# Kernel optimization log

Measured on AMD Instinct MI355X. Metric: run time of the kernel, lower is better.

## Reference

```python
import jax, jax.numpy as jnp
import numpy as np

B, D, E, H, C = 16384, 512, 16, 2048, 1
LN_EPS = 1e-5


def setup_inputs() -> dict:
    key = jax.random.key(0)
    ks = jax.random.split(key, 6)
    scale = 0.02
    return {
        "z": jax.random.normal(ks[0], (B, D), jnp.float32),
        "gate_w": jax.random.normal(ks[1], (D, E), jnp.float32) * scale,
        "gate_b": jnp.zeros((E,), jnp.float32),
        "ln_scale": jnp.ones((E, D), jnp.float32),
        "ln_bias": jnp.zeros((E, D), jnp.float32),
        "w1": jax.random.normal(ks[2], (E, D, H), jnp.float32) * scale,
        "b1": jnp.zeros((E, H), jnp.float32),
        "w2": jax.random.normal(ks[3], (E, H, C), jnp.float32) * scale,
        "b2": jnp.zeros((E, C), jnp.float32),
    }


def reference(z, gate_w, gate_b, ln_scale, ln_bias, w1, b1, w2, b2):
    # Gate: softmax over experts, top-1 routing by argmax
    g = jax.nn.softmax(z @ gate_w + gate_b, axis=-1)  # (B, E)
    idx = jnp.argmax(g, axis=-1)                      # (B,)

    # LayerNorm statistics are expert-independent (affine differs per expert)
    mu = jnp.mean(z, axis=-1, keepdims=True)
    var = jnp.mean(jnp.square(z - mu), axis=-1, keepdims=True)
    zn = (z - mu) / jnp.sqrt(var + LN_EPS)            # (B, D)

    # Loop over the small fixed expert set; combine by top-1 mask.
    logits = jnp.zeros((z.shape[0],), z.dtype)
    for e in range(E):
        x = zn * ln_scale[e] + ln_bias[e]                       # (B, D)
        h = jax.nn.gelu(x @ w1[e] + b1[e], approximate=False)   # (B, H)
        o = jnp.squeeze(h @ w2[e] + b2[e], axis=-1)             # (B,) since C==1
        logits = jnp.where(idx == e, o, logits)
    return logits, g
```

## Files before the change

### kernel.cpp

```cpp
#include <hip/hip_runtime.h>
#include <math.h>

#define NB 16384
#define ND 512
#define NE 16
#define NH 2048
#define BM 128
#define BN 128
#define BK 64
#define NCH (NH / BN)
#define NTB 8
#define LN_EPS 1e-5f

typedef __attribute__((ext_vector_type(8))) short s8v;
typedef __attribute__((ext_vector_type(4))) float f4v;

#define WS_W1T_OFF  ((size_t)0)
#define WS_W1T_BYTES ((size_t)NE * NH * ND * 2)
#define WS_XN_OFF   (WS_W1T_OFF + WS_W1T_BYTES)
#define WS_XN_BYTES ((size_t)NB * ND * 2)
#define WS_IDX_OFF  (WS_XN_OFF + WS_XN_BYTES)
#define WS_CNT_OFF  (WS_IDX_OFF + (size_t)NB * 4)
#define WS_ROWS_OFF (WS_CNT_OFF + 256)

__device__ __forceinline__ unsigned short bf16_rne(float f) {
    unsigned u = __float_as_uint(f);
    unsigned r = (u + 0x7fffu + ((u >> 16) & 1u)) >> 16;
    return (unsigned short)r;
}

__global__ __launch_bounds__(256) void w1conv_kernel(
    const float* __restrict__ w1, unsigned short* __restrict__ w1t)
{
    int bid = blockIdx.x;
    int e = bid & 15;
    int rest = bid >> 4;
    int db = rest & 7;
    int hb = rest >> 3;
    int h = hb * 256 + threadIdx.x;

    const float* src = w1 + ((size_t)e * ND + db * 64) * NH + h;
    unsigned int u[32];
#pragma unroll
    for (int p = 0; p < 32; ++p) {
        float f0 = src[(size_t)(2 * p) * NH];
        float f1 = src[(size_t)(2 * p + 1) * NH];
        u[p] = (unsigned)bf16_rne(f0) | ((unsigned)bf16_rne(f1) << 16);
    }
    uint4* dst = reinterpret_cast<uint4*>(
        w1t + ((size_t)e * NH + h) * ND + db * 64);
#pragma unroll
    for (int p = 0; p < 8; ++p)
        dst[p] = make_uint4(u[4 * p], u[4 * p + 1], u[4 * p + 2], u[4 * p + 3]);
}

__global__ __launch_bounds__(256) void gate_ln_kernel(
    const float* __restrict__ z, const float* __restrict__ gw,
    const float* __restrict__ gb, const float* __restrict__ ln_s,
    const float* __restrict__ ln_b, const float* __restrict__ b2,
    unsigned short* __restrict__ xn, int* __restrict__ idx_ws,
    float* __restrict__ g_out, float* __restrict__ logits)
{
    int wave = threadIdx.x >> 6;
    int lane = threadIdx.x & 63;
    int b = blockIdx.x * 4 + wave;
    int q = lane & 3, dg = lane >> 2;

    const float* zr = z + (size_t)b * ND;
    float4 zv[8];
#pragma unroll
    for (int i = 0; i < 8; ++i)
        zv[i] = *reinterpret_cast<const float4*>(zr + dg * 32 + i * 4);

    float sum = 0.f, ssq = 0.f;
    float ga[4] = {0.f, 0.f, 0.f, 0.f};
#pragma unroll
    for (int i = 0; i < 8; ++i) {
        float zs[4] = {zv[i].x, zv[i].y, zv[i].z, zv[i].w};
#pragma unroll
        for (int t = 0; t < 4; ++t) {
            int d = dg * 32 + i * 4 + t;
            float4 w4 = *reinterpret_cast<const float4*>(gw + (size_t)d * NE + q * 4);
            ga[0] = fmaf(zs[t], w4.x, ga[0]);
            ga[1] = fmaf(zs[t], w4.y, ga[1]);
            ga[2] = fmaf(zs[t], w4.z, ga[2]);
            ga[3] = fmaf(zs[t], w4.w, ga[3]);
            sum += zs[t];
            ssq = fmaf(zs[t], zs[t], ssq);
        }
    }
#pragma unroll
    for (int m = 4; m <= 32; m <<= 1) {
        sum += __shfl_xor(sum, m);
        ssq += __shfl_xor(ssq, m);
#pragma unroll
        for (int j = 0; j < 4; ++j) ga[j] += __shfl_xor(ga[j], m);
    }
#pragma unroll
    for (int j = 0; j < 4; ++j) ga[j] += gb[q * 4 + j];

    float mu = sum * (1.f / ND);
    float var = ssq * (1.f / ND) - mu * mu;
    float rstd = rsqrtf(var + LN_EPS);

    float lmax = fmaxf(fmaxf(ga[0], ga[1]), fmaxf(ga[2], ga[3]));
    lmax = fmaxf(lmax, __shfl_xor(lmax, 1));
    lmax = fmaxf(lmax, __shfl_xor(lmax, 2));
    float ge[4], lsum = 0.f;
#pragma unroll
    for (int j = 0; j < 4; ++j) { ge[j] = __expf(ga[j] - lmax); lsum += ge[j]; }
    lsum += __shfl_xor(lsum, 1);
    lsum += __shfl_xor(lsum, 2);
    float rden = 1.f / lsum;

    int li = 1000;
#pragma unroll
    for (int j = 3; j >= 0; --j) if (ga[j] == lmax) li = q * 4 + j;
    li = min(li, __shfl_xor(li, 1));
    li = min(li, __shfl_xor(li, 2));

    float gv0 = ge[0] * rden, gv1 = ge[1] * rden;
    float gv2 = ge[2] * rden, gv3 = ge[3] * rden;
    int srcl = lane >> 2;
    float t0 = __shfl(gv0, srcl), t1 = __shfl(gv1, srcl);
    float t2 = __shfl(gv2, srcl), t3 = __shfl(gv3, srcl);
    float gval = (q == 0) ? t0 : (q == 1) ? t1 : (q == 2) ? t2 : t3;
    if (lane < NE) g_out[(size_t)b * NE + lane] = gval;

    float4 xa, xc;
    if (q == 0)      { xa = zv[0]; xc = zv[1]; }
    else if (q == 1) { xa = zv[2]; xc = zv[3]; }
    else if (q == 2) { xa = zv[4]; xc = zv[5]; }
    else             { xa = zv[6]; xc = zv[7]; }
    int dofs = dg * 32 + q * 8;
    const float* ls = ln_s + (size_t)li * ND + dofs;
    const float* lb = ln_b + (size_t)li * ND + dofs;
    float4 s0 = *reinterpret_cast<const float4*>(ls);
    float4 s1 = *reinterpret_cast<const float4*>(ls + 4);
    float4 u0 = *reinterpret_cast<const float4*>(lb);
    float4 u1 = *reinterpret_cast<const float4*>(lb + 4);
    unsigned short xb[8];
    xb[0] = bf16_rne((xa.x - mu) * rstd * s0.x + u0.x);
    xb[1] = bf16_rne((xa.y - mu) * rstd * s0.y + u0.y);
    xb[2] = bf16_rne((xa.z - mu) * rstd * s0.z + u0.z);
    xb[3] = bf16_rne((xa.w - mu) * rstd * s0.w + u0.w);
    xb[4] = bf16_rne((xc.x - mu) * rstd * s1.x + u1.x);
    xb[5] = bf16_rne((xc.y - mu) * rstd * s1.y + u1.y);
    xb[6] = bf16_rne((xc.z - mu) * rstd * s1.z + u1.z);
    xb[7] = bf16_rne((xc.w - mu) * rstd * s1.w + u1.w);
    *reinterpret_cast<s8v*>(xn + (size_t)b * ND + dofs) =
        *reinterpret_cast<s8v*>(xb);

    if (lane == 0) {
        idx_ws[b] = li;
        logits[b] = b2[li];
    }
}

__global__ __launch_bounds__(256) void bucket_kernel(
    const int* __restrict__ idx_ws, int* __restrict__ counts,
    int* __restrict__ rows)
{
    __shared__ int qc[4];
    int e = blockIdx.x;
    int tid = threadIdx.x, w = tid >> 6, lane = tid & 63;
    const int4* p = reinterpret_cast<const int4*>(idx_ws) + (size_t)w * 1024;

    int c = 0;
#pragma unroll 4
    for (int it = 0; it < 16; ++it) {
        int4 v = p[it * 64 + lane];
        c += (v.x == e) + (v.y == e) + (v.z == e) + (v.w == e);
    }
#pragma unroll
    for (int m = 1; m < 64; m <<= 1) c += __shfl_xor(c, m);
    if (lane == 0) qc[w] = c;
    __syncthreads();

    int base = 0;
    for (int j = 0; j < w; ++j) base += qc[j];
    unsigned long long below = (lane == 0) ? 0ull : ((~0ull) >> (64 - lane));
    int* re = rows + (size_t)e * NB;
    int run = base;
#pragma unroll 2
    for (int it = 0; it < 16; ++it) {
        int4 v = p[it * 64 + lane];
        int vv[4] = {v.x, v.y, v.z, v.w};
#pragma unroll
        for (int k = 0; k < 4; ++k) {
            unsigned long long m = __ballot(vv[k] == e);
            if (vv[k] == e)
                re[run + __popcll(m & below)] = w * 4096 + (it * 64 + lane) * 4 + k;
            run += __popcll(m);
        }
    }
    if (tid == 0) counts[e] = qc[0] + qc[1] + qc[2] + qc[3];
}

__global__ __launch_bounds__(256, 2) void mfma_mlp(
    const unsigned short* __restrict__ xn, const unsigned short* __restrict__ w1t,
    const float* __restrict__ b1, const float* __restrict__ w2,
    const int* __restrict__ counts, const int* __restrict__ rows,
    float* __restrict__ logits)
{
    __shared__ unsigned short A_lds[2][BM * BK];
    __shared__ unsigned short B_lds[2][BN * BK];

    int bid = blockIdx.x;
    int e = bid & 15;
    int rest = bid >> 4;
    int ch = rest & 15;
    int tb0 = rest >> 4;
    int c0 = ch * BN;
    int tid = threadIdx.x, lane = tid & 63, wave = tid >> 6;
    int wm = wave & 1, wn = wave >> 1;
    int cnt = counts[e];
    const int* rl = rows + (size_t)e * NB;

    int rquad = lane >> 3;
    int sbyte = ((lane & 7) * 16) ^ (rquad << 4);

    size_t boff[4];
#pragma unroll
    for (int i = 0; i < 4; ++i) {
        int cl = (wave * 4 + i) * 8 + rquad;
        boff[i] = ((size_t)(e * NH + c0 + cl) * ND) * 2 + sbyte;
    }

    float b1v[4], w2v[4];
#pragma unroll
    for (int cf = 0; cf < 4; ++cf) {
        int col = c0 + wn * 64 + cf * 16 + (lane & 15);
        b1v[cf] = b1[(size_t)e * NH + col];
        w2v[cf] = w2[(size_t)e * NH + col];
    }

    int g = lane >> 4;
    int fr = lane & 15;
    int sw = (lane & 7) << 4;
    int aoffs[4], boffs[4];
#pragma unroll
    for (int f = 0; f < 4; ++f) {
        aoffs[f] = (wm * 64 + f * 16 + fr) * 128;
        boffs[f] = (wn * 64 + f * 16 + fr) * 128;
    }

    for (int tb = tb0; tb * BM < cnt; tb += NTB) {
        int rbase = tb * BM;

        size_t aoff[4];
#pragma unroll
        for (int i = 0; i < 4; ++i) {
            int rloc = (wave * 4 + i) * 8 + rquad;
            int rg = rl[min(rbase + rloc, cnt - 1)];
            aoff[i] = (size_t)rg * (ND * 2) + sbyte;
        }

#pragma unroll
        for (int i = 0; i < 4; ++i) {
            __builtin_amdgcn_global_load_lds(
                (const __attribute__((address_space(1))) void*)((const char*)xn + aoff[i]),
                (__attribute__((address_space(3))) void*)&A_lds[0][(wave * 4 + i) * 8 * BK],
                16, 0, 0);
            __builtin_amdgcn_global_load_lds(
                (const __attribute__((address_space(1))) void*)((const char*)w1t + boff[i]),
                (__attribute__((address_space(3))) void*)&B_lds[0][(wave * 4 + i) * 8 * BK],
                16, 0, 0);
        }
        __syncthreads();

        f4v acc[4][4];
#pragma unroll
        for (int rf = 0; rf < 4; ++rf)
#pragma unroll
            for (int cf = 0; cf < 4; ++cf) acc[rf][cf] = (f4v){0.f, 0.f, 0.f, 0.f};

#pragma unroll
        for (int s = 0; s < 8; ++s) {
            int cb = s & 1;
            if (s < 7) {
#pragma unroll
                for (int i = 0; i < 4; ++i) {
                    __builtin_amdgcn_global_load_lds(
                        (const __attribute__((address_space(1))) void*)
                            ((const char*)xn + aoff[i] + (s + 1) * 128),
                        (__attribute__((address_space(3))) void*)
                            &A_lds[cb ^ 1][(wave * 4 + i) * 8 * BK],
                        16, 0, 0);
                    __builtin_amdgcn_global_load_lds(
                        (const __attribute__((address_space(1))) void*)
                            ((const char*)w1t + boff[i] + (s + 1) * 128),
                        (__attribute__((address_space(3))) void*)
                            &B_lds[cb ^ 1][(wave * 4 + i) * 8 * BK],
                        16, 0, 0);
                }
            }
#pragma unroll
            for (int ks = 0; ks < 2; ++ks) {
                int kb = (ks * 64 + g * 16) ^ sw;
                s8v a[4], bb[4];
#pragma unroll
                for (int rf = 0; rf < 4; ++rf)
                    a[rf] = *reinterpret_cast<const s8v*>(
                        (const char*)&A_lds[cb][0] + aoffs[rf] + kb);
#pragma unroll
                for (int cf = 0; cf < 4; ++cf)
                    bb[cf] = *reinterpret_cast<const s8v*>(
                        (const char*)&B_lds[cb][0] + boffs[cf] + kb);
#pragma unroll
                for (int rf = 0; rf < 4; ++rf)
#pragma unroll
                    for (int cf = 0; cf < 4; ++cf)
                        acc[rf][cf] = __builtin_amdgcn_mfma_f32_16x16x32_bf16(
                            a[rf], bb[cf], acc[rf][cf], 0, 0, 0);
            }
            if (s < 7) __syncthreads();
        }

#pragma unroll
        for (int rf = 0; rf < 4; ++rf) {
            float pj[4] = {0.f, 0.f, 0.f, 0.f};
#pragma unroll
            for (int cf = 0; cf < 4; ++cf) {
#pragma unroll
                for (int j = 0; j < 4; ++j) {
                    float h = acc[rf][cf][j] + b1v[cf];
                    float uu = h * (0.7978845608f + 0.0356774081f * h * h);
                    float ex = __expf(2.f * uu);
                    float th = 1.f - 2.f / (ex + 1.f);
                    pj[j] = fmaf(0.5f * h * (1.f + th), w2v[cf], pj[j]);
                }
            }
#pragma unroll
            for (int m = 1; m < 16; m <<= 1)
#pragma unroll
                for (int j = 0; j < 4; ++j) pj[j] += __shfl_xor(pj[j], m);
            if ((lane & 15) == 0) {
#pragma unroll
                for (int j = 0; j < 4; ++j) {
                    int rloc = wm * 64 + rf * 16 + g * 4 + j;
                    if (rbase + rloc < cnt)
                        atomicAdd(&logits[rl[rbase + rloc]], pj[j]);
                }
            }
        }
    }
}

extern "C" void kernel_launch(void* const* d_in, const int* in_sizes, int n_in,
                              void* d_out, int out_size, void* d_ws, size_t ws_size,
                              hipStream_t stream) {
    const float* z    = (const float*)d_in[0];
    const float* gw   = (const float*)d_in[1];
    const float* gb   = (const float*)d_in[2];
    const float* ln_s = (const float*)d_in[3];
    const float* ln_b = (const float*)d_in[4];
    const float* w1   = (const float*)d_in[5];
    const float* b1   = (const float*)d_in[6];
    const float* w2   = (const float*)d_in[7];
    const float* b2   = (const float*)d_in[8];

    float* logits = (float*)d_out;
    float* g_out  = (float*)d_out + NB;

    char* ws = (char*)d_ws;
    unsigned short* w1t = (unsigned short*)(ws + WS_W1T_OFF);
    unsigned short* xn  = (unsigned short*)(ws + WS_XN_OFF);
    int* idx_ws = (int*)(ws + WS_IDX_OFF);
    int* cnts   = (int*)(ws + WS_CNT_OFF);
    int* rowl   = (int*)(ws + WS_ROWS_OFF);

    w1conv_kernel<<<NE * 64, 256, 0, stream>>>(w1, w1t);
    gate_ln_kernel<<<NB / 4, 256, 0, stream>>>(z, gw, gb, ln_s, ln_b, b2,
                                               xn, idx_ws, g_out, logits);
    bucket_kernel<<<NE, 256, 0, stream>>>(idx_ws, cnts, rowl);
    mfma_mlp<<<NE * NCH * NTB, 256, 0, stream>>>(xn, w1t, b1, w2, cnts, rowl,
                                                 logits);
}
```

Before: 175.3 us.

## Convert W1 to bf16 inside GEMM and pre-gather rows into contiguous buffer

Drops the separate W1 fp32-to-bf16 transpose kernel. The GEMM now loads fp32 W1 tiles into registers, converts them to bf16 and writes them into swizzled LDS, so the weight tensor is read once instead of being read and re-written. A new gather kernel copies normalized rows into an expert-sorted contiguous buffer, which removes indirect row loads inside the GEMM. The GEMM prefetches across row tiles, blocks with no work exit early, and NTB drops from 8 to 2, so each block covers more row tiles. The cost is redundant fp32 W1 reads and conversions across row-tile blocks, plus one extra gather pass.

```diff
diff --git a/kernel.cpp b/kernel.cpp
--- a/kernel.cpp
+++ b/kernel.cpp
@@ -9,17 +9,17 @@
 #define BN 128
 #define BK 64
 #define NCH (NH / BN)
-#define NTB 8
+#define NTB 2
 #define LN_EPS 1e-5f
 
 typedef __attribute__((ext_vector_type(8))) short s8v;
 typedef __attribute__((ext_vector_type(4))) float f4v;
 
-#define WS_W1T_OFF  ((size_t)0)
-#define WS_W1T_BYTES ((size_t)NE * NH * ND * 2)
-#define WS_XN_OFF   (WS_W1T_OFF + WS_W1T_BYTES)
+#define WS_XN_OFF   ((size_t)0)
 #define WS_XN_BYTES ((size_t)NB * ND * 2)
-#define WS_IDX_OFF  (WS_XN_OFF + WS_XN_BYTES)
+#define WS_XNS_OFF  (WS_XN_OFF + WS_XN_BYTES)
+#define WS_XNS_BYTES ((size_t)NB * ND * 2)
+#define WS_IDX_OFF  (WS_XNS_OFF + WS_XNS_BYTES)
 #define WS_CNT_OFF  (WS_IDX_OFF + (size_t)NB * 4)
 #define WS_ROWS_OFF (WS_CNT_OFF + 256)
 
@@ -28,30 +28,8 @@
     unsigned r = (u + 0x7fffu + ((u >> 16) & 1u)) >> 16;
     return (unsigned short)r;
 }
-
-__global__ __launch_bounds__(256) void w1conv_kernel(
-    const float* __restrict__ w1, unsigned short* __restrict__ w1t)
-{
-    int bid = blockIdx.x;
-    int e = bid & 15;
-    int rest = bid >> 4;
-    int db = rest & 7;
-    int hb = rest >> 3;
-    int h = hb * 256 + threadIdx.x;
-
-    const float* src = w1 + ((size_t)e * ND + db * 64) * NH + h;
-    unsigned int u[32];
-#pragma unroll
-    for (int p = 0; p < 32; ++p) {
-        float f0 = src[(size_t)(2 * p) * NH];
-        float f1 = src[(size_t)(2 * p + 1) * NH];
-        u[p] = (unsigned)bf16_rne(f0) | ((unsigned)bf16_rne(f1) << 16);
-    }
-    uint4* dst = reinterpret_cast<uint4*>(
-        w1t + ((size_t)e * NH + h) * ND + db * 64);
-#pragma unroll
-    for (int p = 0; p < 8; ++p)
-        dst[p] = make_uint4(u[4 * p], u[4 * p + 1], u[4 * p + 2], u[4 * p + 3]);
+__device__ __forceinline__ unsigned int pack2(float a, float b) {
+    return (unsigned)bf16_rne(a) | ((unsigned)bf16_rne(b) << 16);
 }
 
 __global__ __launch_bounds__(256) void gate_ln_kernel(
@@ -197,8 +175,26 @@
     if (tid == 0) counts[e] = qc[0] + qc[1] + qc[2] + qc[3];
 }
 
+__global__ __launch_bounds__(256) void gather_kernel(
+    const unsigned short* __restrict__ xn, const int* __restrict__ counts,
+    const int* __restrict__ rows, unsigned short* __restrict__ xns)
+{
+    int wave = threadIdx.x >> 6, lane = threadIdx.x & 63;
+    int slot = blockIdx.x * 4 + wave;
+
+    int pfx = 0, e = 0;
+#pragma unroll
+    for (int i = 0; i < NE; ++i) {
+        int c = counts[i];
+        if (e == i && slot >= pfx + c) { pfx += c; e = i + 1; }
+    }
+    int row = rows[(size_t)e * NB + (slot - pfx)];
+    s8v v = *reinterpret_cast<const s8v*>(xn + (size_t)row * ND + lane * 8);
+    *reinterpret_cast<s8v*>(xns + (size_t)slot * ND + lane * 8) = v;
+}
+
 __global__ __launch_bounds__(256, 2) void mfma_mlp(
-    const unsigned short* __restrict__ xn, const unsigned short* __restrict__ w1t,
+    const unsigned short* __restrict__ xns, const float* __restrict__ w1,
     const float* __restrict__ b1, const float* __restrict__ w2,
     const int* __restrict__ counts, const int* __restrict__ rows,
     float* __restrict__ logits)
@@ -214,18 +210,19 @@
     int c0 = ch * BN;
     int tid = threadIdx.x, lane = tid & 63, wave = tid >> 6;
     int wm = wave & 1, wn = wave >> 1;
+
     int cnt = counts[e];
+    if (tb0 * BM >= cnt) return;
+    int pfx = 0;
+    for (int i = 0; i < e; ++i) pfx += counts[i];
     const int* rl = rows + (size_t)e * NB;
 
     int rquad = lane >> 3;
     int sbyte = ((lane & 7) * 16) ^ (rquad << 4);
 
-    size_t boff[4];
-#pragma unroll
-    for (int i = 0; i < 4; ++i) {
-        int cl = (wave * 4 + i) * 8 + rquad;
-        boff[i] = ((size_t)(e * NH + c0 + cl) * ND) * 2 + sbyte;
-    }
+    int bc4 = (tid & 31) * 4;
+    int bkq = tid >> 5;
+    const float* bbase = w1 + (size_t)e * ND * NH + c0 + bc4;
 
     float b1v[4], w2v[4];
 #pragma unroll
@@ -245,30 +242,50 @@
         boffs[f] = (wn * 64 + f * 16 + fr) * 128;
     }
 
-    for (int tb = tb0; tb * BM < cnt; tb += NTB) {
+    f4v bfv[8];
+
+#define ISSUE_B(ss)                                                          \
+    {   const float* bs = bbase + (size_t)((ss) * 64 + bkq * 8) * NH;        \
+        _Pragma("unroll")                                                    \
+        for (int j = 0; j < 8; ++j)                                          \
+            bfv[j] = *reinterpret_cast<const f4v*>(bs + (size_t)j * NH); }
+
+#define ISSUE_A(buf, sbase, ss)                                              \
+    {   _Pragma("unroll")                                                    \
+        for (int i = 0; i < 4; ++i) {                                        \
+            int rloc = (wave * 4 + i) * 8 + rquad;                           \
+            int slot = min((sbase) + rloc, NB - 1);                          \
+            __builtin_amdgcn_global_load_lds(                                \
+                (const __attribute__((address_space(1))) void*)              \
+                    ((const char*)xns + (size_t)slot * 1024 + (ss) * 128 + sbyte), \
+                (__attribute__((address_space(3))) void*)                    \
+                    &A_lds[buf][(wave * 4 + i) * 8 * BK], 16, 0, 0); } }
+
+#define WRITE_B(buf)                                                         \
+    {   _Pragma("unroll")                                                    \
+        for (int i = 0; i < 4; ++i) {                                        \
+            int cc = bc4 + i;                                                \
+            int wb = cc * 128 + ((bkq * 16) ^ ((cc & 7) << 4));              \
+            *reinterpret_cast<uint4*>((char*)&B_lds[buf][0] + wb) =          \
+                make_uint4(pack2(bfv[0][i], bfv[1][i]),                      \
+                           pack2(bfv[2][i], bfv[3][i]),                      \
+                           pack2(bfv[4][i], bfv[5][i]),                      \
+                           pack2(bfv[6][i], bfv[7][i])); } }
+
+    int tb = tb0;
+    int sbase = pfx + tb * BM;
+
+    ISSUE_B(0);
+    ISSUE_A(0, sbase, 0);
+    WRITE_B(0);
+    __syncthreads();
+
+    while (true) {
+        int tbn = tb + NTB;
+        bool hasNext = (tbn * BM < cnt);
+        int sbasen = pfx + tbn * BM;
         int rbase = tb * BM;
 
-        size_t aoff[4];
-#pragma unroll
-        for (int i = 0; i < 4; ++i) {
-            int rloc = (wave * 4 + i) * 8 + rquad;
-            int rg = rl[min(rbase + rloc, cnt - 1)];
-            aoff[i] = (size_t)rg * (ND * 2) + sbyte;
-        }
-
-#pragma unroll
-        for (int i = 0; i < 4; ++i) {
-            __builtin_amdgcn_global_load_lds(
-                (const __attribute__((address_space(1))) void*)((const char*)xn + aoff[i]),
-                (__attribute__((address_space(3))) void*)&A_lds[0][(wave * 4 + i) * 8 * BK],
-                16, 0, 0);
-            __builtin_amdgcn_global_load_lds(
-                (const __attribute__((address_space(1))) void*)((const char*)w1t + boff[i]),
-                (__attribute__((address_space(3))) void*)&B_lds[0][(wave * 4 + i) * 8 * BK],
-                16, 0, 0);
-        }
-        __syncthreads();
-
         f4v acc[4][4];
 #pragma unroll
         for (int rf = 0; rf < 4; ++rf)
@@ -276,24 +293,14 @@
             for (int cf = 0; cf < 4; ++cf) acc[rf][cf] = (f4v){0.f, 0.f, 0.f, 0.f};
 
 #pragma unroll
-        for (int s = 0; s < 8; ++s) {
-            int cb = s & 1;
-            if (s < 7) {
-#pragma unroll
-                for (int i = 0; i < 4; ++i) {
-                    __builtin_amdgcn_global_load_lds(
-                        (const __attribute__((address_space(1))) void*)
-                            ((const char*)xn + aoff[i] + (s + 1) * 128),
-                        (__attribute__((address_space(3))) void*)
-                            &A_lds[cb ^ 1][(wave * 4 + i) * 8 * BK],
-                        16, 0, 0);
-                    __builtin_amdgcn_global_load_lds(
-                        (const __attribute__((address_space(1))) void*)
-                            ((const char*)w1t + boff[i] + (s + 1) * 128),
-                        (__attribute__((address_space(3))) void*)
-                            &B_lds[cb ^ 1][(wave * 4 + i) * 8 * BK],
-                        16, 0, 0);
-                }
+        for (int ss = 0; ss < 8; ++ss) {
+            int cb = ss & 1;
+            bool st = (ss < 7) || hasNext;
+            int nss = (ss < 7) ? ss + 1 : 0;
+            int nsb = (ss < 7) ? sbase : sbasen;
+            if (st) {
+                ISSUE_B(nss);
+                ISSUE_A(cb ^ 1, nsb, nss);
             }
 #pragma unroll
             for (int ks = 0; ks < 2; ++ks) {
@@ -314,7 +321,8 @@
                         acc[rf][cf] = __builtin_amdgcn_mfma_f32_16x16x32_bf16(
                             a[rf], bb[cf], acc[rf][cf], 0, 0, 0);
             }
-            if (s < 7) __syncthreads();
+            if (st) WRITE_B(cb ^ 1);
+            __syncthreads();
         }
 
 #pragma unroll
@@ -344,7 +352,14 @@
                 }
             }
         }
-    }
+
+        if (!hasNext) break;
+        tb = tbn;
+        sbase = sbasen;
+    }
+#undef ISSUE_B
+#undef ISSUE_A
+#undef WRITE_B
 }
 
 extern "C" void kernel_launch(void* const* d_in, const int* in_sizes, int n_in,
@@ -364,16 +379,16 @@
     float* g_out  = (float*)d_out + NB;
 
     char* ws = (char*)d_ws;
-    unsigned short* w1t = (unsigned short*)(ws + WS_W1T_OFF);
     unsigned short* xn  = (unsigned short*)(ws + WS_XN_OFF);
+    unsigned short* xns = (unsigned short*)(ws + WS_XNS_OFF);
     int* idx_ws = (int*)(ws + WS_IDX_OFF);
     int* cnts   = (int*)(ws + WS_CNT_OFF);
     int* rowl   = (int*)(ws + WS_ROWS_OFF);
 
-    w1conv_kernel<<<NE * 64, 256, 0, stream>>>(w1, w1t);
     gate_ln_kernel<<<NB / 4, 256, 0, stream>>>(z, gw, gb, ln_s, ln_b, b2,
                                                xn, idx_ws, g_out, logits);
     bucket_kernel<<<NE, 256, 0, stream>>>(idx_ws, cnts, rowl);
-    mfma_mlp<<<NE * NCH * NTB, 256, 0, stream>>>(xn, w1t, b1, w2, cnts, rowl,
+    gather_kernel<<<NB / 4, 256, 0, stream>>>(xn, cnts, rowl, xns);
+    mfma_mlp<<<NE * NCH * NTB, 256, 0, stream>>>(xns, w1, b1, w2, cnts, rowl,
                                                  logits);
 }
```

Measured after the change: 202.6 us. 15.5% more time.
